# Kernel tuning notes

Measured on AMD Instinct MI355X. Metric: run time of the kernel, lower is better.

Reference implementation:

```python
import jax, jax.numpy as jnp
import numpy as np

N, D, NC, K = 4096, 64, 1000, 8192
ALPHA, BETA, GAMMA, SUPT = 0.02, 1.0, 1.0, 1.0
TEMP, BASE_TEMP = 0.05, 0.05
L_INTRA, L_IMEAN, L_IMIN, L_FISHER, EPS = 1.0, 0.1, 0.05, 0.1, 1e-6


def _l2norm(x, axis):
    # torch F.normalize: x / max(||x||, 1e-12)
    n = jnp.sqrt(jnp.sum(x * x, axis=axis, keepdims=True))
    return x / jnp.maximum(n, 1e-12)


def setup_inputs() -> dict:
    key = jax.random.key(0)
    k1, k2, k3, k4, k5 = jax.random.split(key, 5)
    # long-tailed class counts -> log_prior and class_weight buffers
    cls_arr = np.maximum((1280.0 * 0.01 ** (np.arange(NC) / (NC - 1))).astype(np.float32), 1.0)
    prior = cls_arr / cls_arr.sum()
    log_prior = jnp.asarray(np.log(prior), dtype=jnp.float32)
    inv = 1.0 / cls_arr
    class_weight = jnp.asarray((inv / inv.sum() * NC).astype(np.float32))
    feats = jax.random.normal(k1, (N, D), jnp.float32)
    logits = jax.random.normal(k2, (N, NC), jnp.float32)
    labels = jax.random.randint(k3, (N,), 0, NC)
    C = jax.random.normal(k4, (D, NC), jnp.float32) * 0.01  # learnable centers
    queue = jax.random.normal(k5, (K, D), jnp.float32)       # momentum queue buffer
    return {"feats": feats, "logits": logits, "labels": labels, "C": C,
            "queue": queue, "log_prior": log_prior, "class_weight": class_weight}


def reference(feats, logits, labels, C, queue, log_prior, class_weight):
    sg = jax.lax.stop_gradient
    # ---- weighted cross entropy on prior-adjusted logits ----
    sup_logits = (logits + log_prior) / SUPT
    logp = jax.nn.log_softmax(sup_logits, axis=1)
    w = class_weight[labels]
    nll = -jnp.take_along_axis(logp, labels[:, None], axis=1)[:, 0]
    ce_loss = jnp.sum(w * nll) / jnp.sum(w)

    # ---- normalize feats, enqueue (ptr=0, N<=K -> queue[:N] = feats) ----
    f = _l2norm(feats, axis=1)                       # [N, D]
    q = queue.at[:N].set(sg(f))                      # updated queue [K, D]
    centers = _l2norm(C, axis=0).T                   # [NC, D]

    neg_center_sim = f @ centers.T                   # [N, NC]
    neg_queue_sim = f @ q.T                          # [N, K]
    anchor_dot = jnp.concatenate([sg(sup_logits), neg_center_sim, neg_queue_sim], axis=1) / TEMP

    onehot = jax.nn.one_hot(labels, NC, dtype=jnp.float32)  # mask_sup == mask_cent
    mask = jnp.concatenate([onehot * BETA, onehot * ALPHA, jnp.zeros((N, K), jnp.float32)], axis=1)
    logits_mask = jnp.concatenate([jnp.ones((N, 2 * NC), jnp.float32),
                                   jnp.full((N, K), GAMMA, jnp.float32)], axis=1)

    anchor_dot = anchor_dot - sg(jnp.max(anchor_dot, axis=1, keepdims=True))
    exp_logits = jnp.exp(anchor_dot) * logits_mask
    log_prob = anchor_dot - jnp.log(jnp.sum(exp_logits, axis=1, keepdims=True) + 1e-12)
    mean_log_prob_pos = jnp.sum(mask * log_prob, axis=1) / (jnp.sum(mask, axis=1) + 1e-12)
    contrast_loss = -jnp.mean(mean_log_prob_pos) * (TEMP / BASE_TEMP)

    # ---- center regularizers ----
    gram = centers @ centers.T                       # centers are unit-norm rows
    sq = jnp.maximum(2.0 - 2.0 * gram, 1e-12)
    eye = jnp.eye(NC, dtype=bool)
    dist = jnp.sqrt(jnp.where(eye, 1e12, sq))
    dist_no_dg = jnp.where(eye, 1e6, dist)
    inter_min = jnp.min(dist_no_dg)
    inter_mean = jnp.sum(jnp.where(eye, 0.0, dist)) / (NC * (NC - 1))

    diff = f - centers[labels]                       # [N, D]
    intra_d = jnp.mean(jnp.sum(diff * diff, axis=1))
    mu_g = jnp.mean(f, axis=0, keepdims=True)
    cls_cnt = jnp.zeros((NC,), jnp.float32).at[labels].add(1.0)
    S_W = jnp.sum(diff * diff)
    S_B = jnp.sum(jnp.sum((centers - mu_g) ** 2, axis=1) * cls_cnt)
    fisher = S_B / (S_W + EPS)
    reg = (L_INTRA * intra_d + L_IMEAN / (inter_mean + EPS)
           + L_IMIN / (inter_min + EPS) + L_FISHER / (fisher + EPS))
    return ce_loss + contrast_loss + reg
```

## Files before the change

### kernel.cpp

```cpp
#include <hip/hip_runtime.h>
#include <math.h>

#define N_ 4096
#define D_ 64
#define NC_ 1000
#define KQ_ 8192
#define VCOLS 9192
#define VPAD  9216
#define PCH   5
#define TEMP_INV 20.0f
#define M0 20.25f
#define LOG2E 1.4426950408889634f
#define K2L  (TEMP_INV * LOG2E)
#define M0L  (M0 * LOG2E)

#define WS_F     0
#define WS_CENT  (WS_F + N_*D_)
#define WS_SUPM  (WS_CENT + NC_*D_)
#define WS_PSUP  (WS_SUPM + N_)
#define WS_PCENT (WS_PSUP + N_)
#define WS_CEPN  (WS_PCENT + N_)
#define WS_CEPD  (WS_CEPN + 512)
#define WS_CSP   (WS_CEPD + 512)
#define WS_GS    (WS_CSP + 16)
#define WS_GM    (WS_GS + 128)
#define WS_VF    (WS_GM + 128)
#define WS_VC    (WS_VF + 4096)
#define WS_TP    (WS_VC + 4096)
#define WS_CTR   (WS_TP + 64)
#define WS_PS    (WS_CTR + 4)
#define WS_BBF   (WS_PS + N_*PCH)

#define K1_BLOCKS 2058
#define K2_BLOCKS 960
#define K3_BLOCKS 16

typedef __attribute__((ext_vector_type(8))) short short8_t;
typedef __attribute__((ext_vector_type(4))) float f32x4;

__device__ __forceinline__ ushort f2bf(float x) {
    union { float f; unsigned u; } v; v.f = x;
    unsigned r = (v.u + 0x7FFFu + ((v.u >> 16) & 1u)) >> 16;
    return (ushort)r;
}

__device__ __forceinline__ int swz(int byte) {
    return byte ^ (((byte >> 7) & 7) << 4);
}

__device__ __forceinline__ void gload16(const void* g, void* lds) {
    __builtin_amdgcn_global_load_lds(
        (const __attribute__((address_space(1))) unsigned int*)g,
        (__attribute__((address_space(3))) unsigned int*)lds, 16, 0, 0);
}

__global__ __launch_bounds__(256) void k1(const float* __restrict__ feats,
                                          const float* __restrict__ C,
                                          const float* __restrict__ queue,
                                          float* __restrict__ ws,
                                          ushort* __restrict__ B) {
    int b = blockIdx.x;
    int t = threadIdx.x;
    if (b == 0 && t == 0) ((unsigned*)ws)[WS_CTR] = 0u;
    if (b < 1024) {
        int row  = b * 4 + (t >> 6);
        int lane = t & 63;
        float x = feats[row * D_ + lane];
        float ss = x * x;
        #pragma unroll
        for (int m = 32; m >= 1; m >>= 1) ss += __shfl_xor(ss, m, 64);
        float y = x / fmaxf(sqrtf(ss), 1e-12f);
        ws[WS_F + row * D_ + lane] = y;
        B[(size_t)(NC_ + row) * D_ + lane] = f2bf(y);
    } else if (b < 1028) {
        int c = (b - 1024) * 256 + t;
        if (c >= NC_) return;
        float v[D_];
        float ss = 0.0f;
        #pragma unroll
        for (int d = 0; d < D_; ++d) { float x = C[d * NC_ + c]; v[d] = x; ss += x * x; }
        float inv = 1.0f / fmaxf(sqrtf(ss), 1e-12f);
        #pragma unroll
        for (int d = 0; d < D_; ++d) {
            float y = v[d] * inv;
            ws[WS_CENT + c * D_ + d] = y;
            B[(size_t)c * D_ + d] = f2bf(y);
        }
    } else {
        int q = (b - 1028) * 256 + t;
        if (q >= (KQ_ - N_ + 24) * D_) return;
        int r = q >> 6, d = q & 63;
        ushort o = 0;
        if (r < KQ_ - N_) o = f2bf(queue[(size_t)(N_ + r) * D_ + d]);
        B[(size_t)(NC_ + N_ + r) * D_ + d] = o;
    }
}

__global__ __launch_bounds__(256) void k2(const ushort* __restrict__ B,
                                          const float* __restrict__ logits,
                                          const int* __restrict__ labels,
                                          const float* __restrict__ log_prior,
                                          const float* __restrict__ class_weight,
                                          const float* __restrict__ f,
                                          const float* __restrict__ cent,
                                          float* __restrict__ ws) {
    __shared__ char smem[33280];
    int t = threadIdx.x;
    int l = t & 63, w = t >> 6;
    int bid = blockIdx.x;
    int wm = w >> 1, wn = w & 1;
    int lr = l & 15, lg = l >> 4;
    int lk = lg * 8;

    if (bid < 256) {
        char* buf0 = smem;
        char* buf1 = smem + 16384;
        float (*ssum)[2] = (float(*)[2])(smem + 32768);

        int bx = bid & 63, cg = bid >> 6;
        int r0 = bx * 64;
        int cbase = cg * 2304;

        const char* Ag = (const char*)(B + (size_t)(NC_ + r0) * D_);
        #pragma unroll
        for (int j = 0; j < 2; ++j) {
            int seg = w * 2 + j;
            int o = seg * 64 + l;
            int sc = o ^ ((o >> 3) & 7);
            gload16(Ag + sc * 16, buf0 + seg * 1024);
        }
        __syncthreads();
        short8_t a[2][2];
        #pragma unroll
        for (int rf = 0; rf < 2; ++rf) {
            int row = wm * 32 + rf * 16 + lr;
            #pragma unroll
            for (int ks = 0; ks < 2; ++ks)
                a[rf][ks] = *(const short8_t*)(buf0 + swz(row * 128 + ks * 64 + lg * 16));
        }
        __syncthreads();

        int lab[2][4];
        if (cg == 0) {
            #pragma unroll
            for (int rf = 0; rf < 2; ++rf)
                #pragma unroll
                for (int reg = 0; reg < 4; ++reg)
                    lab[rf][reg] = labels[r0 + wm * 32 + rf * 16 + lg * 4 + reg];
        }

        const char* Bg = (const char*)(B + (size_t)cbase * D_);
        auto stageB = [&](int tile, char* buf) {
            const char* Bt = Bg + (size_t)tile * 16384;
            #pragma unroll
            for (int j = 0; j < 4; ++j) {
                int seg = w * 4 + j;
                int o = seg * 64 + l;
                int sc = o ^ ((o >> 3) & 7);
                gload16(Bt + sc * 16, buf + seg * 1024);
            }
        };

        stageB(0, buf0);
        __syncthreads();

        float se[2][4] = {};
        #pragma unroll 2
        for (int it = 0; it < 18; ++it) {
            char* cur = (it & 1) ? buf1 : buf0;
            char* nxt = (it & 1) ? buf0 : buf1;
            if (it < 17) stageB(it + 1, nxt);

            short8_t bfr[4][2];
            #pragma unroll
            for (int cf = 0; cf < 4; ++cf) {
                int col = wn * 64 + cf * 16 + lr;
                #pragma unroll
                for (int ks = 0; ks < 2; ++ks)
                    bfr[cf][ks] = *(const short8_t*)(cur + swz(col * 128 + ks * 64 + lg * 16));
            }

            f32x4 acc[2][4] = {};
            #pragma unroll
            for (int ks = 0; ks < 2; ++ks)
                #pragma unroll
                for (int rf = 0; rf < 2; ++rf)
                    #pragma unroll
                    for (int cf = 0; cf < 4; ++cf)
                        acc[rf][cf] = __builtin_amdgcn_mfma_f32_16x16x32_bf16(
                            a[rf][ks], bfr[cf][ks], acc[rf][cf], 0, 0, 0);

            if (cg == 0 && it < 8) {
                #pragma unroll
                for (int rf = 0; rf < 2; ++rf)
                    #pragma unroll
                    for (int reg = 0; reg < 4; ++reg) {
                        #pragma unroll
                        for (int cf = 0; cf < 4; ++cf) {
                            int col = it * 128 + wn * 64 + cf * 16 + lr;
                            if (col == lab[rf][reg])
                                ws[WS_PCENT + r0 + wm * 32 + rf * 16 + lg * 4 + reg] =
                                    acc[rf][cf][reg];
                        }
                    }
            }

            #pragma unroll
            for (int rf = 0; rf < 2; ++rf)
                #pragma unroll
                for (int cf = 0; cf < 4; ++cf)
                    #pragma unroll
                    for (int reg = 0; reg < 4; ++reg)
                        se[rf][reg] += __builtin_amdgcn_exp2f(
                            fmaf(acc[rf][cf][reg], K2L, -M0L));

            __syncthreads();
        }

        #pragma unroll
        for (int rf = 0; rf < 2; ++rf)
            #pragma unroll
            for (int reg = 0; reg < 4; ++reg) {
                float v = se[rf][reg];
                #pragma unroll
                for (int msk = 1; msk < 16; msk <<= 1)
                    v += __shfl_xor(v, msk, 64);
                if (lr == 0) ssum[wm * 32 + rf * 16 + lg * 4 + reg][wn] = v;
            }
        __syncthreads();
        if (t < 64)
            ws[WS_PS + (size_t)(r0 + t) * PCH + cg] = ssum[t][0] + ssum[t][1];
    } else if (bid < 768) {
        float* lp = (float*)smem;
        float (*cep)[2] = (float(*)[2])(smem + 4096);
        int sid = bid - 256;
        if (t < 250) ((float4*)lp)[t] = ((const float4*)log_prior)[t];
        __syncthreads();
        float cen_acc = 0.0f, ced_acc = 0.0f;
        int rbase = sid * 8 + w * 2;
        #pragma unroll
        for (int rr = 0; rr < 2; ++rr) {
            int row = rbase + rr;
            const float* lrow = logits + (size_t)row * NC_;
            const float4* lrow4 = (const float4*)lrow;
            float vals[16];
            float m = -1e30f;
            #pragma unroll
            for (int it = 0; it < 4; ++it) {
                int idx = it * 64 + l;
                float4 v4 = (idx < 250) ? lrow4[idx]
                                        : make_float4(-1e30f, -1e30f, -1e30f, -1e30f);
                float4 p4 = (idx < 250) ? ((const float4*)lp)[idx]
                                        : make_float4(0, 0, 0, 0);
                vals[it * 4 + 0] = v4.x + p4.x;
                vals[it * 4 + 1] = v4.y + p4.y;
                vals[it * 4 + 2] = v4.z + p4.z;
                vals[it * 4 + 3] = v4.w + p4.w;
                #pragma unroll
                for (int k = 0; k < 4; ++k) m = fmaxf(m, vals[it * 4 + k]);
            }
            #pragma unroll
            for (int msk = 1; msk < 64; msk <<= 1) m = fmaxf(m, __shfl_xor(m, msk, 64));
            float s1 = 0.0f, s20 = 0.0f;
            #pragma unroll
            for (int k = 0; k < 16; ++k) {
                float d = vals[k] - m;
                s1  += __builtin_amdgcn_exp2f(d * LOG2E);
                s20 += __builtin_amdgcn_exp2f(d * K2L);
            }
            #pragma unroll
            for (int msk = 1; msk < 64; msk <<= 1) {
                s1  += __shfl_xor(s1, msk, 64);
                s20 += __shfl_xor(s20, msk, 64);
            }
            if (l == 0) {
                int lab = labels[row];
                float vpos = lrow[lab] + lp[lab];
                float wt = class_weight[lab];
                cen_acc += wt * (m + __logf(s1) - vpos);
                ced_acc += wt;
                ws[WS_SUPM + row] = TEMP_INV * m;
                ws[WS_PS + (size_t)row * PCH + (PCH - 1)] = s20;
                ws[WS_PSUP + row] = TEMP_INV * vpos;
            }
        }
        if (l == 0) { cep[w][0] = cen_acc; cep[w][1] = ced_acc; }
        __syncthreads();
        if (t == 0) {
            ws[WS_CEPN + sid] = cep[0][0] + cep[1][0] + cep[2][0] + cep[3][0];
            ws[WS_CEPD + sid] = cep[0][1] + cep[1][1] + cep[2][1] + cep[3][1];
        }
    } else if (bid < 896) {
        float* gs4 = (float*)smem;
        float* gm4 = gs4 + 4;
        int g = bid - 768;
        int gr = g >> 3, gc = g & 7;
        int r0 = gr * 64 + wm * 32;
        int c0 = gc * 128 + wn * 64;

        const ushort* Af = B + (size_t)(r0 + lr) * D_ + lk;
        const ushort* Bf = B + (size_t)(c0 + lr) * D_ + lk;

        short8_t a[2][2], bfr[4][2];
        #pragma unroll
        for (int rf = 0; rf < 2; ++rf)
            #pragma unroll
            for (int ks = 0; ks < 2; ++ks)
                a[rf][ks] = *(const short8_t*)(Af + rf * 16 * D_ + ks * 32);
        #pragma unroll
        for (int cf = 0; cf < 4; ++cf)
            #pragma unroll
            for (int ks = 0; ks < 2; ++ks)
                bfr[cf][ks] = *(const short8_t*)(Bf + cf * 16 * D_ + ks * 32);

        f32x4 acc[2][4] = {};
        #pragma unroll
        for (int ks = 0; ks < 2; ++ks)
            #pragma unroll
            for (int rf = 0; rf < 2; ++rf)
                #pragma unroll
                for (int cf = 0; cf < 4; ++cf)
                    acc[rf][cf] = __builtin_amdgcn_mfma_f32_16x16x32_bf16(
                        a[rf][ks], bfr[cf][ks], acc[rf][cf], 0, 0, 0);

        float lsum = 0.0f, lmin = 1e30f;
        #pragma unroll
        for (int rf = 0; rf < 2; ++rf)
            #pragma unroll
            for (int cf = 0; cf < 4; ++cf)
                #pragma unroll
                for (int reg = 0; reg < 4; ++reg) {
                    int gi = r0 + rf * 16 + lg * 4 + reg;
                    int gj = c0 + cf * 16 + lr;
                    if (gi < NC_ && gj < NC_ && gi != gj) {
                        float d = sqrtf(fmaxf(2.0f - 2.0f * acc[rf][cf][reg], 1e-12f));
                        lsum += d;
                        lmin = fminf(lmin, d);
                    }
                }
        #pragma unroll
        for (int msk = 1; msk < 64; msk <<= 1) {
            lsum += __shfl_xor(lsum, msk, 64);
            lmin = fminf(lmin, __shfl_xor(lmin, msk, 64));
        }
        if (l == 0) { gs4[w] = lsum; gm4[w] = lmin; }
        __syncthreads();
        if (t == 0) {
            ws[WS_GS + g] = gs4[0] + gs4[1] + gs4[2] + gs4[3];
            ws[WS_GM + g] = fminf(fminf(gm4[0], gm4[1]), fminf(gm4[2], gm4[3]));
        }
    } else {
        float* svf = (float*)smem;
        float* svc = svf + 256;
        float* stp = svc + 256;
        int sb = bid - 896;
        int wid = sb * 4 + w;
        float vf = 0.0f, vc = 0.0f, tacc = 0.0f;
        for (int i = wid; i < N_; i += 256) {
            float x = f[i * D_ + l];
            float c = cent[labels[i] * D_ + l];
            vf += x; vc += c; tacc += x * c;
        }
        #pragma unroll
        for (int msk = 32; msk >= 1; msk >>= 1) tacc += __shfl_xor(tacc, msk, 64);
        svf[w * 64 + l] = vf; svc[w * 64 + l] = vc;
        if (l == 0) stp[w] = tacc;
        __syncthreads();
        if (w == 0) {
            ws[WS_VF + sb * 64 + l] = svf[l] + svf[64 + l] + svf[128 + l] + svf[192 + l];
            ws[WS_VC + sb * 64 + l] = svc[l] + svc[64 + l] + svc[128 + l] + svc[192 + l];
            if (l == 0) ws[WS_TP + sb] = stp[0] + stp[1] + stp[2] + stp[3];
        }
    }
}

__global__ __launch_bounds__(256) void k3(float* __restrict__ ws,
                                          float* __restrict__ out) {
    int t = threadIdx.x;
    int w = t >> 6, l = t & 63;
    int bid = blockIdx.x;
    __shared__ unsigned done;
    __shared__ float cb[4];

    {
        int row = bid * 256 + t;
        const float* pv = ws + WS_PS + (size_t)row * PCH;
        float s = (pv[0] + pv[1]) + (pv[2] + pv[3]);
        float msup = ws[WS_SUPM + row];
        float ssup = pv[PCH - 1];
        float M = fmaxf(M0, msup);
        float stot = s * __builtin_amdgcn_exp2f((M0 - M) * LOG2E)
                   + ssup * __builtin_amdgcn_exp2f((msup - M) * LOG2E);
        float logS = __logf(stot + 1e-12f);
        float lp1 = ws[WS_PSUP + row] - M - logS;
        float lp2 = ws[WS_PCENT + row] * TEMP_INV - M - logS;
        float cacc = (lp1 + 0.02f * lp2) / (1.02f + 1e-12f);
        #pragma unroll
        for (int msk = 1; msk < 64; msk <<= 1) cacc += __shfl_xor(cacc, msk, 64);
        if (l == 0) cb[w] = cacc;
        __syncthreads();
        if (t == 0) ws[WS_CSP + bid] = cb[0] + cb[1] + cb[2] + cb[3];
    }

    __threadfence();
    if (t == 0) done = atomicAdd((unsigned*)ws + WS_CTR, 1u);
    __syncthreads();
    if (done != K3_BLOCKS - 1) return;
    __threadfence();

    float csum = (t < 16) ? ws[WS_CSP + t] : 0.0f;
    float cen = 0.0f, ced = 0.0f;
    #pragma unroll
    for (int k = 0; k < 2; ++k) {
        cen += ws[WS_CEPN + t + k * 256];
        ced += ws[WS_CEPD + t + k * 256];
    }
    float gsum = 0, gmin = 1e30f, vf = 0, vc = 0, tp = 0;
    if (t < 64) {
        tp = ws[WS_TP + t];
        #pragma unroll 8
        for (int b = 0; b < 64; ++b) {
            vf += ws[WS_VF + b * 64 + t];
            vc += ws[WS_VC + b * 64 + t];
        }
    }
    if (t < 128) { gsum = ws[WS_GS + t]; gmin = ws[WS_GM + t]; }
    float mu_d = vf * (1.0f / (float)N_);
    float vmu  = vc * mu_d;
    float mumu = mu_d * mu_d;
    #pragma unroll
    for (int m = 32; m >= 1; m >>= 1) {
        csum += __shfl_xor(csum, m, 64);
        cen  += __shfl_xor(cen, m, 64);
        ced  += __shfl_xor(ced, m, 64);
        gsum += __shfl_xor(gsum, m, 64);
        gmin = fminf(gmin, __shfl_xor(gmin, m, 64));
        vmu  += __shfl_xor(vmu, m, 64);
        mumu += __shfl_xor(mumu, m, 64);
        tp   += __shfl_xor(tp, m, 64);
    }
    __shared__ float red[4][8];
    if (l == 0) {
        red[w][0] = csum; red[w][1] = cen; red[w][2] = ced; red[w][3] = gsum;
        red[w][4] = gmin; red[w][5] = vmu; red[w][6] = mumu; red[w][7] = tp;
    }
    __syncthreads();
    if (t == 0) {
        float CSM = red[0][0] + red[1][0] + red[2][0] + red[3][0];
        float CEN = red[0][1] + red[1][1] + red[2][1] + red[3][1];
        float CED = red[0][2] + red[1][2] + red[2][2] + red[3][2];
        float GSM = red[0][3] + red[1][3] + red[2][3] + red[3][3];
        float GMN = fminf(fminf(red[0][4], red[1][4]), fminf(red[2][4], red[3][4]));
        float VMU = red[0][5] + red[1][5] + red[2][5] + red[3][5];
        float MUMU = red[0][6] + red[1][6] + red[2][6] + red[3][6];
        float T   = red[0][7] + red[1][7] + red[2][7] + red[3][7];
        float SW = 2.0f * (float)N_ - 2.0f * T;
        float SB = (float)N_ - 2.0f * VMU + (float)N_ * MUMU;
        float intra = SW / (float)N_;
        float fisher = SB / (SW + 1e-6f);
        float ce = CEN / CED;
        float contrast = -(CSM / (float)N_);
        float inter_mean = GSM / (float)(NC_ * (NC_ - 1));
        float reg = intra + 0.1f / (inter_mean + 1e-6f)
                  + 0.05f / (GMN + 1e-6f) + 0.1f / (fisher + 1e-6f);
        out[0] = ce + contrast + reg;
    }
}

extern "C" void kernel_launch(void* const* d_in, const int* in_sizes, int n_in,
                              void* d_out, int out_size, void* d_ws, size_t ws_size,
                              hipStream_t stream) {
    const float* feats        = (const float*)d_in[0];
    const float* logits       = (const float*)d_in[1];
    const int*   labels       = (const int*)d_in[2];
    const float* C            = (const float*)d_in[3];
    const float* queue        = (const float*)d_in[4];
    const float* log_prior    = (const float*)d_in[5];
    const float* class_weight = (const float*)d_in[6];
    float* ws  = (float*)d_ws;
    float* out = (float*)d_out;
    ushort* Bbf = (ushort*)(ws + WS_BBF);

    hipLaunchKernelGGL(k1, dim3(K1_BLOCKS), dim3(256), 0, stream,
                       feats, C, queue, ws, Bbf);
    hipLaunchKernelGGL(k2, dim3(K2_BLOCKS), dim3(256), 0, stream,
                       Bbf, logits, labels, log_prior, class_weight,
                       ws + WS_F, ws + WS_CENT, ws);
    hipLaunchKernelGGL(k3, dim3(K3_BLOCKS), dim3(256), 0, stream, ws, out);
}
```

Before: 40.11 us.

## Triple-buffer B tiles with vmcnt-based waits and register-held center picks

Moves the GEMM-plus-exp loop from double to triple buffering in LDS, prefetching two tiles ahead. Waits use explicit s_waitcnt vmcnt(4) plus raw s_barrier in place of a full __syncthreads, so one load group can stay in flight across iterations. The positive-center logit is now kept in registers with a hit flag and written once after the loop, removing the per-iteration conditional global store. LDS use grows to about 48KB per block, which may reduce occupancy, and every block now loads labels and runs the compare/select each iteration.

```diff
diff --git a/kernel.cpp b/kernel.cpp
--- a/kernel.cpp
+++ b/kernel.cpp
@@ -104,7 +104,7 @@
                                           const float* __restrict__ f,
                                           const float* __restrict__ cent,
                                           float* __restrict__ ws) {
-    __shared__ char smem[33280];
+    __shared__ char smem[49664];
     int t = threadIdx.x;
     int l = t & 63, w = t >> 6;
     int bid = blockIdx.x;
@@ -113,9 +113,10 @@
     int lk = lg * 8;
 
     if (bid < 256) {
-        char* buf0 = smem;
-        char* buf1 = smem + 16384;
-        float (*ssum)[2] = (float(*)[2])(smem + 32768);
+        char* bufA = smem;
+        char* bufB = smem + 16384;
+        char* bufC = smem + 32768;
+        float (*ssum)[2] = (float(*)[2])(smem + 49152);
 
         int bx = bid & 63, cg = bid >> 6;
         int r0 = bx * 64;
@@ -127,7 +128,7 @@
             int seg = w * 2 + j;
             int o = seg * 64 + l;
             int sc = o ^ ((o >> 3) & 7);
-            gload16(Ag + sc * 16, buf0 + seg * 1024);
+            gload16(Ag + sc * 16, bufC + seg * 1024);
         }
         __syncthreads();
         short8_t a[2][2];
@@ -136,18 +137,16 @@
             int row = wm * 32 + rf * 16 + lr;
             #pragma unroll
             for (int ks = 0; ks < 2; ++ks)
-                a[rf][ks] = *(const short8_t*)(buf0 + swz(row * 128 + ks * 64 + lg * 16));
+                a[rf][ks] = *(const short8_t*)(bufC + swz(row * 128 + ks * 64 + lg * 16));
         }
         __syncthreads();
 
         int lab[2][4];
-        if (cg == 0) {
-            #pragma unroll
-            for (int rf = 0; rf < 2; ++rf)
-                #pragma unroll
-                for (int reg = 0; reg < 4; ++reg)
-                    lab[rf][reg] = labels[r0 + wm * 32 + rf * 16 + lg * 4 + reg];
-        }
+        #pragma unroll
+        for (int rf = 0; rf < 2; ++rf)
+            #pragma unroll
+            for (int reg = 0; reg < 4; ++reg)
+                lab[rf][reg] = labels[r0 + wm * 32 + rf * 16 + lg * 4 + reg];
 
         const char* Bg = (const char*)(B + (size_t)cbase * D_);
         auto stageB = [&](int tile, char* buf) {
@@ -161,15 +160,18 @@
             }
         };
 
-        stageB(0, buf0);
-        __syncthreads();
-
         float se[2][4] = {};
-        #pragma unroll 2
-        for (int it = 0; it < 18; ++it) {
-            char* cur = (it & 1) ? buf1 : buf0;
-            char* nxt = (it & 1) ? buf0 : buf1;
-            if (it < 17) stageB(it + 1, nxt);
+        float pc[2][4] = {};
+        int   hit[2][4] = {};
+
+        stageB(0, bufA);
+        stageB(1, bufB);
+        asm volatile("s_waitcnt vmcnt(4)" ::: "memory");
+        __builtin_amdgcn_s_barrier();
+        __builtin_amdgcn_sched_barrier(0);
+
+        auto step = [&](char* cur, char* nxt, int it) {
+            if (it < 16) stageB(it + 2, nxt);
 
             short8_t bfr[4][2];
             #pragma unroll
@@ -190,20 +192,18 @@
                         acc[rf][cf] = __builtin_amdgcn_mfma_f32_16x16x32_bf16(
                             a[rf][ks], bfr[cf][ks], acc[rf][cf], 0, 0, 0);
 
-            if (cg == 0 && it < 8) {
-                #pragma unroll
-                for (int rf = 0; rf < 2; ++rf)
+            #pragma unroll
+            for (int rf = 0; rf < 2; ++rf)
+                #pragma unroll
+                for (int reg = 0; reg < 4; ++reg) {
                     #pragma unroll
-                    for (int reg = 0; reg < 4; ++reg) {
-                        #pragma unroll
-                        for (int cf = 0; cf < 4; ++cf) {
-                            int col = it * 128 + wn * 64 + cf * 16 + lr;
-                            if (col == lab[rf][reg])
-                                ws[WS_PCENT + r0 + wm * 32 + rf * 16 + lg * 4 + reg] =
-                                    acc[rf][cf][reg];
-                        }
+                    for (int cf = 0; cf < 4; ++cf) {
+                        int gcol = cbase + it * 128 + wn * 64 + cf * 16 + lr;
+                        bool m = (gcol == lab[rf][reg]);
+                        pc[rf][reg]  = m ? acc[rf][cf][reg] : pc[rf][reg];
+                        hit[rf][reg] = m ? 1 : hit[rf][reg];
                     }
-            }
+                }
 
             #pragma unroll
             for (int rf = 0; rf < 2; ++rf)
@@ -214,8 +214,27 @@
                         se[rf][reg] += __builtin_amdgcn_exp2f(
                             fmaf(acc[rf][cf][reg], K2L, -M0L));
 
-            __syncthreads();
-        }
+            if (it < 16) {
+                asm volatile("s_waitcnt vmcnt(4)" ::: "memory");
+            } else {
+                asm volatile("s_waitcnt vmcnt(0)" ::: "memory");
+            }
+            __builtin_amdgcn_s_barrier();
+            __builtin_amdgcn_sched_barrier(0);
+        };
+
+        for (int ms = 0; ms < 6; ++ms) {
+            step(bufA, bufC, ms * 3 + 0);
+            step(bufB, bufA, ms * 3 + 1);
+            step(bufC, bufB, ms * 3 + 2);
+        }
+
+        #pragma unroll
+        for (int rf = 0; rf < 2; ++rf)
+            #pragma unroll
+            for (int reg = 0; reg < 4; ++reg)
+                if (hit[rf][reg])
+                    ws[WS_PCENT + r0 + wm * 32 + rf * 16 + lg * 4 + reg] = pc[rf][reg];
 
         #pragma unroll
         for (int rf = 0; rf < 2; ++rf)
```

Result: slower. 51.08 us (+27.3%).
